# Kernel tuning notes

Hardware: AMD Instinct MI355X
Metric: run time of the kernel (lower is better)

## Reference

```python
import jax, jax.numpy as jnp
import numpy as np

NUM_HEADS = 16
HEAD_DIM = 64
COMP_RATIO = 8


def setup_inputs() -> dict:
    key = jax.random.key(0)
    ks = jax.random.split(key, 6)
    d_model = NUM_HEADS * HEAD_DIM  # 1024
    B, S = 2, 8192
    scale = 1.0 / np.sqrt(d_model)
    x = jax.random.normal(ks[0], (B, S, d_model), dtype=jnp.float32)
    Wq = jax.random.normal(ks[1], (d_model, NUM_HEADS * HEAD_DIM), dtype=jnp.float32) * scale
    Wk = jax.random.normal(ks[2], (d_model, NUM_HEADS * HEAD_DIM), dtype=jnp.float32) * scale
    Wv = jax.random.normal(ks[3], (d_model, NUM_HEADS * HEAD_DIM), dtype=jnp.float32) * scale
    Wo = jax.random.normal(ks[4], (NUM_HEADS * HEAD_DIM, d_model), dtype=jnp.float32) * scale
    bq = jnp.zeros((NUM_HEADS * HEAD_DIM,), jnp.float32)
    bk = jnp.zeros((NUM_HEADS * HEAD_DIM,), jnp.float32)
    bv = jnp.zeros((NUM_HEADS * HEAD_DIM,), jnp.float32)
    bo = jnp.zeros((d_model,), jnp.float32)
    return {"x": x, "local_window_start": 4096, "Wq": Wq, "bq": bq,
            "Wk": Wk, "bk": bk, "Wv": Wv, "bv": bv, "Wo": Wo, "bo": bo}


def reference(x, local_window_start, Wq, bq, Wk, bk, Wv, bv, Wo, bo):
    B, S, D = x.shape
    H, Hd, R = NUM_HEADS, HEAD_DIM, COMP_RATIO
    if local_window_start <= R:
        return jnp.zeros_like(x)
    num_pools = local_window_start // R
    if num_pools == 0:
        return jnp.zeros_like(x)
    trunc = num_pools * R
    # avg-pool compression of tokens before the local window
    compressed = x[:, :trunc, :].reshape(B, num_pools, R, D).mean(axis=2)  # (B, P, D)
    # projections
    q = (x @ Wq + bq).reshape(B, S, H, Hd).transpose(0, 2, 1, 3)            # (B,H,S,Hd)
    k = (compressed @ Wk + bk).reshape(B, num_pools, H, Hd).transpose(0, 2, 1, 3)  # (B,H,P,Hd)
    v = (compressed @ Wv + bv).reshape(B, num_pools, H, Hd).transpose(0, 2, 1, 3)
    scale = 1.0 / jnp.sqrt(jnp.float32(Hd))
    scores = jnp.einsum('bhqd,bhkd->bhqk', q, k) * scale                    # (B,H,S,P)
    # causal mask: a query can attend to a pool only if the pool fully precedes it
    q_pos = jnp.arange(S)[:, None]
    pool_end = (jnp.arange(num_pools) + 1) * R
    mask = q_pos >= pool_end[None, :]                                       # (S, P)
    scores = jnp.where(mask[None, None], scores, -1e9)
    attn = jax.nn.softmax(scores, axis=-1)
    out = jnp.einsum('bhqk,bhkd->bhqd', attn, v)                            # (B,H,S,Hd)
    out = out.transpose(0, 2, 1, 3).reshape(B, S, H * Hd)
    return out @ Wo + bo
```

## Files before the change

kernel.cpp:

```cpp
#include <hip/hip_runtime.h>
#include <hip/hip_bf16.h>


typedef __attribute__((ext_vector_type(8))) short bf16x8;
typedef __attribute__((ext_vector_type(4))) short bf16x4;
typedef __attribute__((ext_vector_type(4))) float f32x4;

#define MFMA_BF16(a, b, c) __builtin_amdgcn_mfma_f32_16x16x32_bf16((a), (b), (c), 0, 0, 0)

__device__ __forceinline__ unsigned short f2bu(float x) {
  __hip_bfloat16 b = __float2bfloat16(x);
  return __builtin_bit_cast(unsigned short, b);
}

__device__ __forceinline__ unsigned cvtpk(float lo, float hi) {
  unsigned r;
  asm("v_cvt_pk_bf16_f32 %0, %1, %2" : "=v"(r) : "v"(lo), "v"(hi));
  return r;
}

__device__ __forceinline__ float fexp2(float x) {
  float r;
  asm("v_exp_f32 %0, %1" : "=v"(r) : "v"(x));
  return r;
}

__device__ __forceinline__ void gload_lds16(const void* g, void* l) {
  __builtin_amdgcn_global_load_lds(
      (const __attribute__((address_space(1))) unsigned*)(g),
      (__attribute__((address_space(3))) unsigned*)(l), 16, 0, 0);
}

__device__ __forceinline__ unsigned ldsaddr(const void* p) {
  return (unsigned)(unsigned long long)(const __attribute__((address_space(3))) char*)p;
}

__global__ void prep_kernel(const float* __restrict__ x,
                            __hip_bfloat16* __restrict__ xb,
                            __hip_bfloat16* __restrict__ cb,
                            const float* __restrict__ w0, const float* __restrict__ w1,
                            const float* __restrict__ w2, const float* __restrict__ w3,
                            __hip_bfloat16* __restrict__ t0, __hip_bfloat16* __restrict__ t1,
                            __hip_bfloat16* __restrict__ t2, __hip_bfloat16* __restrict__ t3) {
  __shared__ float tile[32][33];
  const int bid = blockIdx.x;
  const int tid = threadIdx.x;
  if (bid < 2048) {
    const int b = bid >> 10, g = bid & 1023;
    const int d = tid * 4;
    const size_t rb = ((size_t)(b * 8192 + g * 8)) * 1024 + d;
    float4 a = {0.f, 0.f, 0.f, 0.f};
#pragma unroll
    for (int r = 0; r < 8; ++r) {
      const float4 v = *(const float4*)&x[rb + (size_t)r * 1024];
      ushort4 o;
      o.x = f2bu(v.x); o.y = f2bu(v.y); o.z = f2bu(v.z); o.w = f2bu(v.w);
      *(ushort4*)&xb[rb + (size_t)r * 1024] = o;
      a.x += v.x; a.y += v.y; a.z += v.z; a.w += v.w;
    }
    if (g < 512) {
      ushort4 o;
      o.x = f2bu(a.x * 0.125f); o.y = f2bu(a.y * 0.125f);
      o.z = f2bu(a.z * 0.125f); o.w = f2bu(a.w * 0.125f);
      *(ushort4*)&cb[((size_t)(b * 512 + g)) * 1024 + d] = o;
    }
  } else {
    const int t = bid - 2048;
    const int z = t >> 10, rem = t & 1023;
    const int k0 = (rem & 31) * 32, n0 = (rem >> 5) * 32;
    const float* W; __hip_bfloat16* T;
    switch (z) {
      case 0: W = w0; T = t0; break;
      case 1: W = w1; T = t1; break;
      case 2: W = w2; T = t2; break;
      default: W = w3; T = t3; break;
    }
    const int tx = tid & 31, ty = tid >> 5;
#pragma unroll
    for (int j = 0; j < 4; ++j) {
      const int kk = ty + j * 8;
      tile[kk][tx] = W[(size_t)(k0 + kk) * 1024 + n0 + tx];
    }
    __syncthreads();
#pragma unroll
    for (int j = 0; j < 4; ++j) {
      const int nn = ty + j * 8;
      T[(size_t)(n0 + nn) * 1024 + k0 + tx] = __float2bfloat16(tile[tx][nn]);
    }
  }
}


#define STAGE(SPTR, SROWBASE, STILE, SLDSOFF)                                  \
  {                                                                            \
    const int _t = (STILE) < NT ? (STILE) : 0;                                 \
    const size_t _kb = (size_t)_t * 128;                                       \
    gload_lds16((const char*)(SPTR) + ((size_t)((SROWBASE) + srow0) * K) * 2 + _kb + scb0, \
                ldsC + (SLDSOFF) + wave * 1024);                               \
    gload_lds16((const char*)(SPTR) + ((size_t)((SROWBASE) + srow0 + 64) * K) * 2 + _kb + scb0, \
                ldsC + (SLDSOFF) + 8192 + wave * 1024);                        \
  }

#define MM4(MR, AF0, AF1)                                                      \
  acc[MR][0] = MFMA_BF16(AF0, bf00, acc[MR][0]);                               \
  acc[MR][1] = MFMA_BF16(AF0, bf10, acc[MR][1]);                               \
  acc[MR][2] = MFMA_BF16(AF0, bf20, acc[MR][2]);                               \
  acc[MR][3] = MFMA_BF16(AF0, bf30, acc[MR][3]);                               \
  acc[MR][0] = MFMA_BF16(AF1, bf01, acc[MR][0]);                               \
  acc[MR][1] = MFMA_BF16(AF1, bf11, acc[MR][1]);                               \
  acc[MR][2] = MFMA_BF16(AF1, bf21, acc[MR][2]);                               \
  acc[MR][3] = MFMA_BF16(AF1, bf31, acc[MR][3]);

#define PHASE(QM, DB, LOADB, SPTR, SROWBASE, STILE, SLDSOFF, DOVM)             \
  {                                                                            \
    bf16x8 af0, af1, af2, af3;                                                 \
    const unsigned ab = Ab0 + (DB)*32768u + (QM)*4096u;                        \
    asm volatile("ds_read_b128 %0, %1" : "=v"(af0) : "v"(ab));                 \
    asm volatile("ds_read_b128 %0, %1" : "=v"(af1) : "v"(ab ^ 64u));           \
    asm volatile("ds_read_b128 %0, %1" : "=v"(af2) : "v"(ab + 2048u));         \
    asm volatile("ds_read_b128 %0, %1" : "=v"(af3) : "v"((ab + 2048u) ^ 64u)); \
    if (LOADB) {                                                               \
      const unsigned bb = Bb0 + (DB)*32768u;                                   \
      asm volatile("ds_read_b128 %0, %1" : "=v"(bf00) : "v"(bb));              \
      asm volatile("ds_read_b128 %0, %1" : "=v"(bf01) : "v"(bb ^ 64u));        \
      asm volatile("ds_read_b128 %0, %1" : "=v"(bf10) : "v"(bb + 2048u));      \
      asm volatile("ds_read_b128 %0, %1" : "=v"(bf11) : "v"((bb + 2048u) ^ 64u)); \
      asm volatile("ds_read_b128 %0, %1" : "=v"(bf20) : "v"(bb + 4096u));      \
      asm volatile("ds_read_b128 %0, %1" : "=v"(bf21) : "v"((bb + 4096u) ^ 64u)); \
      asm volatile("ds_read_b128 %0, %1" : "=v"(bf30) : "v"(bb + 6144u));      \
      asm volatile("ds_read_b128 %0, %1" : "=v"(bf31) : "v"((bb + 6144u) ^ 64u)); \
    }                                                                          \
    STAGE(SPTR, SROWBASE, STILE, SLDSOFF)                                      \
    asm volatile("s_barrier" ::: "memory");                                    \
    asm volatile("s_waitcnt lgkmcnt(0)" ::: "memory");                         \
    __builtin_amdgcn_sched_barrier(0);                                         \
    __builtin_amdgcn_s_setprio(1);                                             \
    MM4((QM)*2 + 0, af0, af1)                                                  \
    MM4((QM)*2 + 1, af2, af3)                                                  \
    __builtin_amdgcn_s_setprio(0);                                             \
    if (DOVM) asm volatile("s_waitcnt vmcnt(4)" ::: "memory");                 \
    asm volatile("s_barrier" ::: "memory");                                    \
  }

template <typename OUT_T>
__global__ __launch_bounds__(512, 2) void gemm256_kernel(
    const __hip_bfloat16* __restrict__ A, const __hip_bfloat16* __restrict__ Bt,
    const float* __restrict__ bias, OUT_T* __restrict__ C, int M, int N, int K,
    float oscale) {
  __shared__ alignas(16) char lds[131072];
  char* ldsC = lds;
  const int tid = threadIdx.x;
  const int wave = tid >> 6, lane = tid & 63;
  const int l15 = lane & 15, lg = lane >> 4;
  const int wm = wave >> 2, wn = wave & 3;

  const int nwg = gridDim.x, cpx = nwg >> 3;
  const int bid = blockIdx.x;
  const int swz = (bid & 7) * cpx + (bid >> 3);
  const int ncol = N >> 8;
  const int bn = swz % ncol, bm = swz / ncol;
  const long brow = (long)bm * 256;
  const long bcol = (long)bn * 256;

  const int NT = K >> 6;
  const int NITER = K >> 7;

  const int o0 = wave * 1024 + lane * 16;
  const int srow0 = o0 >> 7;
  const int scb0 = (o0 & 127) ^ ((srow0 & 7) << 4);

  const unsigned LB = ldsaddr(lds);
  const int off0 = (lg * 16) ^ ((l15 & 7) << 4);
  const unsigned Ab0 = LB + wm * 16384u + l15 * 128u + off0;
  const unsigned Bb0 = LB + 65536u + (wn >> 1) * 16384u + (wn & 1) * 8192u + l15 * 128u + off0;

  f32x4 acc[8][4];
#pragma unroll
  for (int m = 0; m < 8; ++m)
#pragma unroll
    for (int n = 0; n < 4; ++n) acc[m][n] = (f32x4){0.f, 0.f, 0.f, 0.f};

  bf16x8 bf00, bf01, bf10, bf11, bf20, bf21, bf30, bf31;

  STAGE(Bt, bcol + 128, 0, 81920)
  STAGE(Bt, bcol,       0, 65536)
  STAGE(A,  brow,       0, 0)
  STAGE(A,  brow + 128, 0, 16384)
  STAGE(Bt, bcol + 128, 1, 114688)
  STAGE(Bt, bcol,       1, 98304)
  asm volatile("s_waitcnt vmcnt(4)" ::: "memory");
  asm volatile("s_barrier" ::: "memory");

  for (int i = 0; i < NITER; ++i) {
    const int t0 = 2 * i;
    PHASE(0, 0, true,  A,  brow,       t0 + 1, 32768,  false)
    PHASE(1, 0, false, A,  brow + 128, t0 + 1, 49152,  false)
    PHASE(2, 0, false, Bt, bcol + 128, t0 + 2, 81920,  false)
    PHASE(3, 0, false, Bt, bcol,       t0 + 2, 65536,  true)
    PHASE(0, 1, true,  A,  brow,       t0 + 2, 0,      false)
    PHASE(1, 1, false, A,  brow + 128, t0 + 2, 16384,  false)
    PHASE(2, 1, false, Bt, bcol + 128, t0 + 3, 114688, false)
    PHASE(3, 1, false, Bt, bcol,       t0 + 3, 98304,  true)
  }

#pragma unroll
  for (int nn = 0; nn < 4; ++nn) {
    const long col = bcol + wn * 64 + nn * 16 + l15;
    const float bv = bias[col];
#pragma unroll
    for (int mr = 0; mr < 8; ++mr) {
      const long row = brow + wm * 128 + mr * 16 + lg * 4;
#pragma unroll
      for (int j = 0; j < 4; ++j) {
        const float v = (acc[mr][nn][j] + bv) * oscale;
        if constexpr (sizeof(OUT_T) == 2)
          C[(row + j) * N + col] = __float2bfloat16(v);
        else
          C[(row + j) * N + col] = v;
      }
    }
  }
}

__global__ __launch_bounds__(256, 2) void gemm_bt_dual_kernel(
    const __hip_bfloat16* __restrict__ A,
    const __hip_bfloat16* __restrict__ Bt0, const float* __restrict__ b0,
    __hip_bfloat16* __restrict__ C0,
    const __hip_bfloat16* __restrict__ Bt1, const float* __restrict__ b1,
    __hip_bfloat16* __restrict__ Vt, int M, int N, int K) {
  const int sel = blockIdx.x >= 16;
  const __hip_bfloat16* Bt = sel ? Bt1 : Bt0;
  const float* bias = sel ? b1 : b0;
  const int bx = blockIdx.x - (sel ? 16 : 0);

  __shared__ alignas(16) __hip_bfloat16 As[128 * 32];
  __shared__ alignas(16) __hip_bfloat16 Bs[64 * 32];
  const int tid = threadIdx.x;
  const int wave = tid >> 6, lane = tid & 63;
  const int l15 = lane & 15, lg = lane >> 4;
  const long brow = (long)blockIdx.y * 128;
  const long bcol = (long)bx * 64;
  const int wr = (wave >> 1) * 64;
  const int wc = (wave & 1) * 32;

  f32x4 acc[4][2];
#pragma unroll
  for (int m = 0; m < 4; ++m)
#pragma unroll
    for (int n = 0; n < 2; ++n) acc[m][n] = (f32x4){0.f, 0.f, 0.f, 0.f};

  for (int kt = 0; kt < K; kt += 32) {
#pragma unroll
    for (int j = 0; j < 2; ++j) {
      const int seg = wave * 2 + j;
      const int o = seg * 1024;
      const int ob = o + lane * 16;
      const int row = ob >> 6;
      const int cb = ob & 63;
      gload_lds16((const char*)A + ((brow + row) * (long)K + kt) * 2 + cb, (char*)As + o);
    }
    if (wave < 4) {
      const int o = wave * 1024;
      const int ob = o + lane * 16;
      const int row = ob >> 6;
      const int cb = ob & 63;
      gload_lds16((const char*)Bt + ((bcol + row) * (long)K + kt) * 2 + cb, (char*)Bs + o);
    }
    __syncthreads();
    bf16x8 af[4], bfr[2];
#pragma unroll
    for (int m = 0; m < 4; ++m)
      af[m] = *(const bf16x8*)&As[(wr + m * 16 + l15) * 32 + lg * 8];
#pragma unroll
    for (int n = 0; n < 2; ++n)
      bfr[n] = *(const bf16x8*)&Bs[(wc + n * 16 + l15) * 32 + lg * 8];
#pragma unroll
    for (int m = 0; m < 4; ++m)
#pragma unroll
      for (int n = 0; n < 2; ++n)
        acc[m][n] = MFMA_BF16(af[m], bfr[n], acc[m][n]);
    __syncthreads();
  }

#pragma unroll
  for (int m = 0; m < 4; ++m)
#pragma unroll
    for (int n = 0; n < 2; ++n) {
      const long col = bcol + wc + n * 16 + l15;
      const float bv = bias[col];
      const long row0 = brow + wr + m * 16 + lg * 4;
      if (!sel) {
#pragma unroll
        for (int r = 0; r < 4; ++r)
          C0[(row0 + r) * N + col] = __float2bfloat16(acc[m][n][r] + bv);
      } else {
        const int bb = (int)(row0 >> 9);
        const int p = (int)(row0 & 511);
        ushort4 w;
        w.x = f2bu(acc[m][n][0] + bv);
        w.y = f2bu(acc[m][n][1] + bv);
        w.z = f2bu(acc[m][n][2] + bv);
        w.w = f2bu(acc[m][n][3] + bv);
        *(ushort4*)&Vt[((size_t)(bb * 1024 + col)) * 512 + p] = w;
      }
    }
}

__global__ __launch_bounds__(512, 2) void attn_kernel(
    const __hip_bfloat16* __restrict__ Q,
    const __hip_bfloat16* __restrict__ Km,
    const __hip_bfloat16* __restrict__ Vt,
    __hip_bfloat16* __restrict__ O) {
  __shared__ alignas(16) __hip_bfloat16 Ks[512 * 64];
  __shared__ alignas(16) __hip_bfloat16 VT[64 * 512];
  const int bh = blockIdx.x;
  const int b = bh >> 4, h = bh & 15;
  const int tid = threadIdx.x, wave = tid >> 6, lane = tid & 63;
  const int l15 = lane & 15, lg = lane >> 4;
  const char* Kbase = (const char*)(Km + (size_t)b * 512 * 1024 + h * 64);
  const char* VtP = (const char*)(Vt + (size_t)bh * 32768);
  char* KsB = (char*)Ks;
  char* VTB = (char*)VT;

#pragma unroll
  for (int j = 0; j < 8; ++j) {
    const int seg = wave * 8 + j;
    const int p = seg * 8 + (lane >> 3);
    const int cb = ((lane & 7) * 16) ^ ((p & 7) << 4);
    gload_lds16(Kbase + (size_t)p * 2048 + cb, KsB + seg * 1024);
  }
#pragma unroll
  for (int j = 0; j < 8; ++j) {
    const int d = wave * 8 + j;
    const int cb = (lane * 16) ^ ((d & 7) << 4);
    gload_lds16(VtP + (size_t)d * 1024 + cb, VTB + d * 1024);
  }
  __syncthreads();

  const short one_bf = (short)0x3F80;
  const bf16x8 ones = {one_bf, one_bf, one_bf, one_bf,
                       one_bf, one_bf, one_bf, one_bf};

  for (int itq = 0; itq < 4; ++itq) {
    const int y = blockIdx.y;
    const int sidx = (itq == 0) ? y : (itq == 1) ? 15 - y
                   : (itq == 2) ? 16 + y : 31 - y;
    const int q0 = sidx * 256 + wave * 32;
    const __hip_bfloat16* Qr0 = Q + ((size_t)(b * 8192 + q0 + l15)) * 1024 + h * 64;
    const __hip_bfloat16* Qr1 = Qr0 + (size_t)16 * 1024;
    const bf16x8 qa0 = *(const bf16x8*)(Qr0 + lg * 8);
    const bf16x8 qa1 = *(const bf16x8*)(Qr0 + 32 + lg * 8);
    const bf16x8 qb0 = *(const bf16x8*)(Qr1 + lg * 8);
    const bf16x8 qb1 = *(const bf16x8*)(Qr1 + 32 + lg * 8);

    f32x4 lac0 = {0.f, 0.f, 0.f, 0.f}, lac1 = {0.f, 0.f, 0.f, 0.f};
    f32x4 o4[2][4];
#pragma unroll
    for (int g = 0; g < 2; ++g)
#pragma unroll
      for (int d = 0; d < 4; ++d) o4[g][d] = (f32x4){0.f, 0.f, 0.f, 0.f};

#pragma unroll
    for (int ch = 0; ch < 4; ++ch) {
      if (!(ch == 0 || q0 == 0 || q0 >= ch * 1024)) continue;

      f32x4 s[2][8];
#pragma unroll
      for (int cc = 0; cc < 8; ++cc) {
        const int p = ch * 128 + cc * 16 + l15;
        const int rb = p * 128;
        const int sw = (p & 7) << 4;
        const bf16x8 kf0 = *(const bf16x8*)(KsB + rb + ((lg * 16) ^ sw));
        const bf16x8 kf1 = *(const bf16x8*)(KsB + rb + ((lg * 16 + 64) ^ sw));
        f32x4 z0 = {0.f, 0.f, 0.f, 0.f};
        z0 = MFMA_BF16(kf0, qa0, z0);
        z0 = MFMA_BF16(kf1, qa1, z0);
        s[0][cc] = z0;
        f32x4 z1 = {0.f, 0.f, 0.f, 0.f};
        z1 = MFMA_BF16(kf0, qb0, z1);
        z1 = MFMA_BF16(kf1, qb1, z1);
        s[1][cc] = z1;
      }
      if (q0 < (ch + 1) * 1024) {
#pragma unroll
        for (int g = 0; g < 2; ++g) {
          const int qa = q0 + g * 16 + l15;
          const float mval = (qa >= 8) ? -1.0e9f : 0.f;
#pragma unroll
          for (int cc = 0; cc < 8; ++cc) {
            const int pb8 = (ch * 128 + cc * 16 + lg * 4 + 1) * 8;
#pragma unroll
            for (int r = 0; r < 4; ++r)
              if (qa < pb8 + r * 8) s[g][cc][r] = mval;
          }
        }
      }
#pragma unroll
      for (int cc = 0; cc < 8; ++cc)
#pragma unroll
        for (int r = 0; r < 4; ++r) {
          s[0][cc][r] = fexp2(s[0][cc][r]);
          s[1][cc][r] = fexp2(s[1][cc][r]);
        }
#pragma unroll
      for (int kc = 0; kc < 4; ++kc) {
        uint4 u0, u1;
        u0.x = cvtpk(s[0][kc * 2][0], s[0][kc * 2][1]);
        u0.y = cvtpk(s[0][kc * 2][2], s[0][kc * 2][3]);
        u0.z = cvtpk(s[0][kc * 2 + 1][0], s[0][kc * 2 + 1][1]);
        u0.w = cvtpk(s[0][kc * 2 + 1][2], s[0][kc * 2 + 1][3]);
        u1.x = cvtpk(s[1][kc * 2][0], s[1][kc * 2][1]);
        u1.y = cvtpk(s[1][kc * 2][2], s[1][kc * 2][3]);
        u1.z = cvtpk(s[1][kc * 2 + 1][0], s[1][kc * 2 + 1][1]);
        u1.w = cvtpk(s[1][kc * 2 + 1][2], s[1][kc * 2 + 1][3]);
        const bf16x8 p0 = __builtin_bit_cast(bf16x8, u0);
        const bf16x8 p1 = __builtin_bit_cast(bf16x8, u1);
        lac0 = MFMA_BF16(ones, p0, lac0);
        lac1 = MFMA_BF16(ones, p1, lac1);
        const int pbase = ch * 128 + kc * 32;
#pragma unroll
        for (int db = 0; db < 4; ++db) {
          const int d = db * 16 + l15;
          const int rowb = d * 1024;
          const int sw = (d & 7) << 4;
          const bf16x4 v0 = *(const bf16x4*)(VTB + rowb + (((pbase + lg * 4) * 2) ^ sw));
          const bf16x4 v1 = *(const bf16x4*)(VTB + rowb + (((pbase + 16 + lg * 4) * 2) ^ sw));
          const bf16x8 af = {v0[0], v0[1], v0[2], v0[3], v1[0], v1[1], v1[2], v1[3]};
          o4[0][db] = MFMA_BF16(af, p0, o4[0][db]);
          o4[1][db] = MFMA_BF16(af, p1, o4[1][db]);
        }
      }
    }
#pragma unroll
    for (int g = 0; g < 2; ++g) {
      const float inv = 1.f / (g ? lac1[0] : lac0[0]);
      __hip_bfloat16* Op =
          O + ((size_t)(b * 8192 + q0 + g * 16 + l15)) * 1024 + h * 64 + lg * 4;
#pragma unroll
      for (int db = 0; db < 4; ++db) {
        uint2 w;
        w.x = cvtpk(o4[g][db][0] * inv, o4[g][db][1] * inv);
        w.y = cvtpk(o4[g][db][2] * inv, o4[g][db][3] * inv);
        *(uint2*)(Op + db * 16) = w;
      }
    }
  }
}

extern "C" void kernel_launch(void* const* d_in, const int* in_sizes, int n_in,
                              void* d_out, int out_size, void* d_ws, size_t ws_size,
                              hipStream_t stream) {
  const float* x  = (const float*)d_in[0];
  const float* Wq = (const float*)d_in[2];
  const float* bq = (const float*)d_in[3];
  const float* Wk = (const float*)d_in[4];
  const float* bk = (const float*)d_in[5];
  const float* Wv = (const float*)d_in[6];
  const float* bv = (const float*)d_in[7];
  const float* Wo = (const float*)d_in[8];
  const float* bo = (const float*)d_in[9];
  float* out = (float*)d_out;

  constexpr size_t SZ_XB = (size_t)16384 * 1024 * 2;
  constexpr size_t SZ_WT = (size_t)1024 * 1024 * 2;
  constexpr size_t SZ_CB = (size_t)1024 * 1024 * 2;
  char* ws = (char*)d_ws;
  __hip_bfloat16* xb   = (__hip_bfloat16*)ws;
  __hip_bfloat16* WqT  = (__hip_bfloat16*)(ws + SZ_XB);
  __hip_bfloat16* WkT  = (__hip_bfloat16*)(ws + SZ_XB + SZ_WT);
  __hip_bfloat16* WvT  = (__hip_bfloat16*)(ws + SZ_XB + 2 * SZ_WT);
  __hip_bfloat16* WoT  = (__hip_bfloat16*)(ws + SZ_XB + 3 * SZ_WT);
  __hip_bfloat16* cbuf = (__hip_bfloat16*)(ws + SZ_XB + 4 * SZ_WT);
  __hip_bfloat16* Qb   = (__hip_bfloat16*)(ws + SZ_XB + 4 * SZ_WT + SZ_CB);
  __hip_bfloat16* Kb   = (__hip_bfloat16*)(ws + SZ_XB + 4 * SZ_WT + SZ_CB + SZ_XB);
  __hip_bfloat16* Vtb  = (__hip_bfloat16*)(ws + SZ_XB + 4 * SZ_WT + SZ_CB + SZ_XB + SZ_CB);

  constexpr float SC = 0.18033688011112042f;

  prep_kernel<<<dim3(6144), dim3(256), 0, stream>>>(
      x, xb, cbuf, Wq, Wk, Wv, Wo, WqT, WkT, WvT, WoT);
  gemm256_kernel<__hip_bfloat16><<<dim3(256), dim3(512), 0, stream>>>(
      xb, WqT, bq, Qb, 16384, 1024, 1024, SC);
  gemm_bt_dual_kernel<<<dim3(32, 8), dim3(256), 0, stream>>>(
      cbuf, WkT, bk, Kb, WvT, bv, Vtb, 1024, 1024, 1024);
  attn_kernel<<<dim3(32, 8), dim3(512), 0, stream>>>(Qb, Kb, Vtb, xb);
  gemm256_kernel<float><<<dim3(256), dim3(512), 0, stream>>>(
      xb, WoT, bo, out, 16384, 1024, 1024, 1.0f);
}
```

Measured before the change: 157.2 us.

## Replace 256x256 GEMM tile with 128x256 tile and K=32 stages

The Q and output projection GEMMs move from a 256x256 block tile with 64-wide K stages to a 128x256 tile with 32-wide K stages. Each stage now covers two matrix rows per 128-byte LDS line under a new swizzle. LDS use drops from 128KB to 48KB and the grid doubles to 512 workgroups. The aim is better occupancy and load balance across the CUs, at the cost of lower arithmetic intensity per tile and more barriers per unit of K.

```diff
diff --git a/kernel.cpp b/kernel.cpp
--- a/kernel.cpp
+++ b/kernel.cpp
@@ -91,63 +91,54 @@
 }
 
 
-#define STAGE(SPTR, SROWBASE, STILE, SLDSOFF)                                  \
+#define SG_A(STILE, DBUF)                                                      \
   {                                                                            \
     const int _t = (STILE) < NT ? (STILE) : 0;                                 \
-    const size_t _kb = (size_t)_t * 128;                                       \
-    gload_lds16((const char*)(SPTR) + ((size_t)((SROWBASE) + srow0) * K) * 2 + _kb + scb0, \
-                ldsC + (SLDSOFF) + wave * 1024);                               \
-    gload_lds16((const char*)(SPTR) + ((size_t)((SROWBASE) + srow0 + 64) * K) * 2 + _kb + scb0, \
-                ldsC + (SLDSOFF) + 8192 + wave * 1024);                        \
-  }
-
-#define MM4(MR, AF0, AF1)                                                      \
-  acc[MR][0] = MFMA_BF16(AF0, bf00, acc[MR][0]);                               \
-  acc[MR][1] = MFMA_BF16(AF0, bf10, acc[MR][1]);                               \
-  acc[MR][2] = MFMA_BF16(AF0, bf20, acc[MR][2]);                               \
-  acc[MR][3] = MFMA_BF16(AF0, bf30, acc[MR][3]);                               \
-  acc[MR][0] = MFMA_BF16(AF1, bf01, acc[MR][0]);                               \
-  acc[MR][1] = MFMA_BF16(AF1, bf11, acc[MR][1]);                               \
-  acc[MR][2] = MFMA_BF16(AF1, bf21, acc[MR][2]);                               \
-  acc[MR][3] = MFMA_BF16(AF1, bf31, acc[MR][3]);
-
-#define PHASE(QM, DB, LOADB, SPTR, SROWBASE, STILE, SLDSOFF, DOVM)             \
+    gload_lds16((const char*)A + (size_t)(brow + row0) * K2 + _t * 64 + kb0,   \
+                ldsC + (DBUF) * 8192 + wave * 1024);                           \
+  }
+
+#define SG_B(STILE, DBUF, LINE)                                                \
   {                                                                            \
-    bf16x8 af0, af1, af2, af3;                                                 \
-    const unsigned ab = Ab0 + (DB)*32768u + (QM)*4096u;                        \
-    asm volatile("ds_read_b128 %0, %1" : "=v"(af0) : "v"(ab));                 \
-    asm volatile("ds_read_b128 %0, %1" : "=v"(af1) : "v"(ab ^ 64u));           \
-    asm volatile("ds_read_b128 %0, %1" : "=v"(af2) : "v"(ab + 2048u));         \
-    asm volatile("ds_read_b128 %0, %1" : "=v"(af3) : "v"((ab + 2048u) ^ 64u)); \
+    const int _t = (STILE) < NT ? (STILE) : 0;                                 \
+    gload_lds16((const char*)Bt + (size_t)(bcol + row0 + (LINE) * 128) * K2 +  \
+                    _t * 64 + kb0,                                             \
+                ldsC + 16384 + (DBUF) * 16384 + (LINE) * 8192 + wave * 1024);  \
+  }
+
+#define PH(MR, DB, LOADB, SKIND, STILE, SDB, SLINE, DOVM)                      \
+  {                                                                            \
+    bf16x8 af;                                                                 \
+    const unsigned ab = Ab0 + (DB)*8192u + (MR)*1024u;                         \
+    asm volatile("ds_read_b128 %0, %1" : "=v"(af) : "v"(ab));                  \
     if (LOADB) {                                                               \
-      const unsigned bb = Bb0 + (DB)*32768u;                                   \
-      asm volatile("ds_read_b128 %0, %1" : "=v"(bf00) : "v"(bb));              \
-      asm volatile("ds_read_b128 %0, %1" : "=v"(bf01) : "v"(bb ^ 64u));        \
-      asm volatile("ds_read_b128 %0, %1" : "=v"(bf10) : "v"(bb + 2048u));      \
-      asm volatile("ds_read_b128 %0, %1" : "=v"(bf11) : "v"((bb + 2048u) ^ 64u)); \
-      asm volatile("ds_read_b128 %0, %1" : "=v"(bf20) : "v"(bb + 4096u));      \
-      asm volatile("ds_read_b128 %0, %1" : "=v"(bf21) : "v"((bb + 4096u) ^ 64u)); \
-      asm volatile("ds_read_b128 %0, %1" : "=v"(bf30) : "v"(bb + 6144u));      \
-      asm volatile("ds_read_b128 %0, %1" : "=v"(bf31) : "v"((bb + 6144u) ^ 64u)); \
+      const unsigned bb = Bb0 + (DB)*16384u;                                   \
+      asm volatile("ds_read_b128 %0, %1" : "=v"(bf0) : "v"(bb));               \
+      asm volatile("ds_read_b128 %0, %1" : "=v"(bf1) : "v"(bb + 1024u));       \
+      asm volatile("ds_read_b128 %0, %1" : "=v"(bf2) : "v"(bb + 2048u));       \
+      asm volatile("ds_read_b128 %0, %1" : "=v"(bf3) : "v"(bb + 3072u));       \
     }                                                                          \
-    STAGE(SPTR, SROWBASE, STILE, SLDSOFF)                                      \
+    if ((SKIND) == 1) SG_A(STILE, SDB)                                         \
+    if ((SKIND) == 2) SG_B(STILE, SDB, SLINE)                                  \
     asm volatile("s_barrier" ::: "memory");                                    \
     asm volatile("s_waitcnt lgkmcnt(0)" ::: "memory");                         \
     __builtin_amdgcn_sched_barrier(0);                                         \
     __builtin_amdgcn_s_setprio(1);                                             \
-    MM4((QM)*2 + 0, af0, af1)                                                  \
-    MM4((QM)*2 + 1, af2, af3)                                                  \
+    acc[MR][0] = MFMA_BF16(af, bf0, acc[MR][0]);                               \
+    acc[MR][1] = MFMA_BF16(af, bf1, acc[MR][1]);                               \
+    acc[MR][2] = MFMA_BF16(af, bf2, acc[MR][2]);                               \
+    acc[MR][3] = MFMA_BF16(af, bf3, acc[MR][3]);                               \
     __builtin_amdgcn_s_setprio(0);                                             \
-    if (DOVM) asm volatile("s_waitcnt vmcnt(4)" ::: "memory");                 \
+    if (DOVM) asm volatile("s_waitcnt vmcnt(2)" ::: "memory");                 \
     asm volatile("s_barrier" ::: "memory");                                    \
   }
 
 template <typename OUT_T>
-__global__ __launch_bounds__(512, 2) void gemm256_kernel(
+__global__ __launch_bounds__(512, 2) void gemm8p_kernel(
     const __hip_bfloat16* __restrict__ A, const __hip_bfloat16* __restrict__ Bt,
     const float* __restrict__ bias, OUT_T* __restrict__ C, int M, int N, int K,
     float oscale) {
-  __shared__ alignas(16) char lds[131072];
+  __shared__ alignas(16) char lds[49152];
   char* ldsC = lds;
   const int tid = threadIdx.x;
   const int wave = tid >> 6, lane = tid & 63;
@@ -159,48 +150,51 @@
   const int swz = (bid & 7) * cpx + (bid >> 3);
   const int ncol = N >> 8;
   const int bn = swz % ncol, bm = swz / ncol;
-  const long brow = (long)bm * 256;
+  const long brow = (long)bm * 128;
   const long bcol = (long)bn * 256;
 
-  const int NT = K >> 6;
-  const int NITER = K >> 7;
+  const int NT = K >> 5;
+  const int NITER = K >> 6;
+  const int K2 = K * 2;
 
   const int o0 = wave * 1024 + lane * 16;
-  const int srow0 = o0 >> 7;
-  const int scb0 = (o0 & 127) ^ ((srow0 & 7) << 4);
+  const int Lr0 = o0 >> 7;
+  const int x0 = (o0 & 127) ^ ((Lr0 & 7) << 4);
+  const int row0 = 2 * Lr0 + (x0 >> 6);
+  const int kb0 = x0 & 63;
 
   const unsigned LB = ldsaddr(lds);
-  const int off0 = (lg * 16) ^ ((l15 & 7) << 4);
-  const unsigned Ab0 = LB + wm * 16384u + l15 * 128u + off0;
-  const unsigned Bb0 = LB + 65536u + (wn >> 1) * 16384u + (wn & 1) * 8192u + l15 * 128u + off0;
-
-  f32x4 acc[8][4];
-#pragma unroll
-  for (int m = 0; m < 8; ++m)
+  const int swzr = ((l15 >> 1) & 7) << 4;
+  const int intra = (((l15 & 1) * 64) + lg * 16) ^ swzr;
+  const unsigned Ab0 = LB + wm * 4096u + (l15 >> 1) * 128u + intra;
+  const unsigned Bb0 = LB + 16384u + wn * 4096u + (l15 >> 1) * 128u + intra;
+
+  f32x4 acc[4][4];
+#pragma unroll
+  for (int m = 0; m < 4; ++m)
 #pragma unroll
     for (int n = 0; n < 4; ++n) acc[m][n] = (f32x4){0.f, 0.f, 0.f, 0.f};
 
-  bf16x8 bf00, bf01, bf10, bf11, bf20, bf21, bf30, bf31;
-
-  STAGE(Bt, bcol + 128, 0, 81920)
-  STAGE(Bt, bcol,       0, 65536)
-  STAGE(A,  brow,       0, 0)
-  STAGE(A,  brow + 128, 0, 16384)
-  STAGE(Bt, bcol + 128, 1, 114688)
-  STAGE(Bt, bcol,       1, 98304)
-  asm volatile("s_waitcnt vmcnt(4)" ::: "memory");
+  bf16x8 bf0, bf1, bf2, bf3;
+
+  SG_A(0, 0)
+  SG_B(0, 0, 0)
+  SG_B(0, 0, 1)
+  SG_B(1, 1, 0)
+  SG_B(1, 1, 1)
+  asm volatile("s_waitcnt vmcnt(2)" ::: "memory");
   asm volatile("s_barrier" ::: "memory");
 
   for (int i = 0; i < NITER; ++i) {
     const int t0 = 2 * i;
-    PHASE(0, 0, true,  A,  brow,       t0 + 1, 32768,  false)
-    PHASE(1, 0, false, A,  brow + 128, t0 + 1, 49152,  false)
-    PHASE(2, 0, false, Bt, bcol + 128, t0 + 2, 81920,  false)
-    PHASE(3, 0, false, Bt, bcol,       t0 + 2, 65536,  true)
-    PHASE(0, 1, true,  A,  brow,       t0 + 2, 0,      false)
-    PHASE(1, 1, false, A,  brow + 128, t0 + 2, 16384,  false)
-    PHASE(2, 1, false, Bt, bcol + 128, t0 + 3, 114688, false)
-    PHASE(3, 1, false, Bt, bcol,       t0 + 3, 98304,  true)
+    PH(0, 0, true,  1, t0 + 1, 1, 0, false)
+    PH(1, 0, false, 2, t0 + 2, 0, 0, false)
+    PH(2, 0, false, 2, t0 + 2, 0, 1, false)
+    PH(3, 0, false, 0, 0, 0, 0,       true)
+    PH(0, 1, true,  1, t0 + 2, 0, 0, false)
+    PH(1, 1, false, 2, t0 + 3, 1, 0, false)
+    PH(2, 1, false, 2, t0 + 3, 1, 1, false)
+    PH(3, 1, false, 0, 0, 0, 0,       true)
   }
 
 #pragma unroll
@@ -208,8 +202,8 @@
     const long col = bcol + wn * 64 + nn * 16 + l15;
     const float bv = bias[col];
 #pragma unroll
-    for (int mr = 0; mr < 8; ++mr) {
-      const long row = brow + wm * 128 + mr * 16 + lg * 4;
+    for (int mr = 0; mr < 4; ++mr) {
+      const long row = brow + wm * 64 + mr * 16 + lg * 4;
 #pragma unroll
       for (int j = 0; j < 4; ++j) {
         const float v = (acc[mr][nn][j] + bv) * oscale;
@@ -479,11 +473,11 @@
 
   prep_kernel<<<dim3(6144), dim3(256), 0, stream>>>(
       x, xb, cbuf, Wq, Wk, Wv, Wo, WqT, WkT, WvT, WoT);
-  gemm256_kernel<__hip_bfloat16><<<dim3(256), dim3(512), 0, stream>>>(
+  gemm8p_kernel<__hip_bfloat16><<<dim3(512), dim3(512), 0, stream>>>(
       xb, WqT, bq, Qb, 16384, 1024, 1024, SC);
   gemm_bt_dual_kernel<<<dim3(32, 8), dim3(256), 0, stream>>>(
       cbuf, WkT, bk, Kb, WvT, bv, Vtb, 1024, 1024, 1024);
   attn_kernel<<<dim3(32, 8), dim3(512), 0, stream>>>(Qb, Kb, Vtb, xb);
-  gemm256_kernel<float><<<dim3(256), dim3(512), 0, stream>>>(
+  gemm8p_kernel<float><<<dim3(512), dim3(512), 0, stream>>>(
       xb, WoT, bo, out, 16384, 1024, 1024, 1.0f);
 }
```

New measurement: 161.1 us. 2.5% more time.
